# Kernel optimization log

Hardware: AMD Instinct MI355X
Metric: run time of the kernel (lower is better)

## Reference

```python
import jax, jax.numpy as jnp
import numpy as np

B = 16384
NUM_V = 1024
NUM_H = 1024
HYPER_DIM = 64
K = 10  # gibbs steps
T = 1.0


def setup_inputs() -> dict:
    key = jax.random.key(0)
    ks = jax.random.split(key, 9)
    v_data = jax.random.bernoulli(ks[0], 0.5, (B, NUM_V)).astype(jnp.float32)
    cond = jax.random.uniform(ks[1], (B, 1), jnp.float32)
    W = 0.01 * jax.random.normal(ks[2], (NUM_V, NUM_H), jnp.float32)
    b = 0.01 * jax.random.normal(ks[3], (NUM_V,), jnp.float32)
    c = 0.01 * jax.random.normal(ks[4], (NUM_H,), jnp.float32)
    fc1_w = jax.random.normal(ks[5], (HYPER_DIM, 1), jnp.float32)
    fc1_b = jnp.zeros((HYPER_DIM,), jnp.float32)
    fc2_w = jax.random.normal(ks[6], (2 * (NUM_V + NUM_H), HYPER_DIM), jnp.float32) / np.sqrt(HYPER_DIM)
    fc2_b = jnp.zeros((2 * (NUM_V + NUM_H),), jnp.float32)
    return {"v_data": v_data, "cond": cond, "W": W, "b": b, "c": c,
            "fc1_w": fc1_w, "fc1_b": fc1_b, "fc2_w": fc2_w, "fc2_b": fc2_b}


def _mod_biases(cond, b, c, fc1_w, fc1_b, fc2_w, fc2_b):
    x = jnp.tanh(cond @ fc1_w.T + fc1_b)
    y = x @ fc2_w.T + fc2_b  # [B, 2*(num_v+num_h)]
    gamma_b, beta_b, gamma_c, beta_c = jnp.split(
        y, [NUM_V, 2 * NUM_V, 2 * NUM_V + NUM_H], axis=-1)
    b_mod = (1.0 + gamma_b) * b[None, :] + beta_b  # [B, num_v]
    c_mod = (1.0 + gamma_c) * c[None, :] + beta_c  # [B, num_h]
    return b_mod, c_mod


def _free_energy(v, W, b_mod, c_mod):
    vW = v @ W  # [B, num_h]
    W_colsum = W.sum(axis=0)  # [num_h]
    sp_normal = jax.nn.softplus(vW + c_mod).sum(axis=-1)
    sp_flipped = jax.nn.softplus(W_colsum[None, :] - vW + c_mod).sum(axis=-1)
    vb_normal = -(v * b_mod).sum(axis=-1)
    vb_flipped = -((1.0 - v) * b_mod).sum(axis=-1)
    F_normal = vb_normal - sp_normal
    F_flipped = vb_flipped - sp_flipped
    negF = jnp.stack([-F_normal, -F_flipped], axis=-1)
    return -T * jax.nn.logsumexp(negF / T, axis=-1)


def _gibbs_step(carry, step_key, W, b_mod, c_mod):
    v, u = carry
    kh, ku, kv = jax.random.split(step_key, 3)
    v_branch = u * v + (1.0 - u) * (1.0 - v)
    p_h = jax.nn.sigmoid((v_branch @ W + c_mod) / T)
    h = jax.random.bernoulli(kh, p_h).astype(v.dtype)
    a = h @ W.T  # [B, num_v]
    dE = (-b_mod.sum(axis=-1) - a.sum(axis=-1)
          + 2.0 * (v * b_mod).sum(axis=-1) + 2.0 * (v * a).sum(axis=-1))
    p_u = jax.nn.sigmoid(dE / T)
    u = jax.random.bernoulli(ku, p_u).astype(v.dtype)[:, None]
    p_v = jax.nn.sigmoid((a + b_mod) / T)
    v_branch_new = jax.random.bernoulli(kv, p_v).astype(v.dtype)
    v_next = u * v_branch_new + (1.0 - u) * (1.0 - v_branch_new)
    return (v_next, u), None


def reference(v_data, cond, W, b, c, fc1_w, fc1_b, fc2_w, fc2_b):
    b_mod, c_mod = _mod_biases(cond, b, c, fc1_w, fc1_b, fc2_w, fc2_b)
    Bn = v_data.shape[0]
    key = jax.random.key(42)
    k_u, k_chain = jax.random.split(key)
    u0 = jax.random.bernoulli(k_u, 0.5, (Bn, 1)).astype(v_data.dtype)
    step_keys = jax.random.split(k_chain, K)
    step = lambda carry, sk: _gibbs_step(carry, sk, W, b_mod, c_mod)
    (v_model, _), _ = jax.lax.scan(step, (v_data, u0), step_keys)
    v_model = jax.lax.stop_gradient(v_model)
    loss = (_free_energy(v_data, W, b_mod, c_mod).mean()
            - _free_energy(v_model, W, b_mod, c_mod).mean())
    return loss
```

## Files before the change

### kernel.cpp

```cpp
#include <hip/hip_runtime.h>
#include <hip/hip_bf16.h>
#include <stdint.h>


#define NB 16384
#define KSTEPS 10
#define LDA 1152
#define KD 1088
#define NT 17
#define SLS 136
#define USALT 4000u
#define ONE8 ((unsigned char)0x38)

typedef __attribute__((ext_vector_type(4))) float f32x4;
typedef __attribute__((ext_vector_type(4))) unsigned int u32x4;

__device__ __forceinline__ unsigned hash32(unsigned idx, unsigned salt) {
  unsigned x = idx + salt * 0x9E3779B9u;
  x = (x ^ (x >> 16)) * 0x7feb352du;
  x = (x ^ (x >> 15)) * 0x846ca68bu;
  return x ^ (x >> 16);
}
__device__ __forceinline__ float rng_u01(unsigned salt, unsigned idx) {
  return (float)(hash32(idx, salt) >> 8) * (1.0f / 16777216.0f);
}
__device__ __forceinline__ float sigm(float z) { return 1.0f / (1.0f + __expf(-z)); }
__device__ __forceinline__ float softplus_(float z) {
  return fmaxf(z, 0.f) + __logf(1.f + __expf(-fabsf(z)));
}
__device__ __forceinline__ float lse2(float a, float b) {
  float m = fmaxf(a, b);
  return m + log1pf(__expf(fminf(a, b) - m));
}
__device__ __forceinline__ float bf2f(unsigned short s) {
  unsigned u = ((unsigned)s) << 16;
  return *reinterpret_cast<float*>(&u);
}
__device__ __forceinline__ unsigned short f2bf(float f) {
  __hip_bfloat16 h = __float2bfloat16(f);
  return *reinterpret_cast<unsigned short*>(&h);
}
__device__ unsigned char f2e4m3(float f) {
  unsigned u = __float_as_uint(f);
  unsigned char s = (unsigned char)((u >> 24) & 0x80);
  float af = fabsf(f);
  if (af >= 448.f) return s | 0x7E;
  float sub = rintf(af * 512.f);
  if (sub < 1.f) return s;
  if (af < 0.015625f) {
    int m = (int)sub;
    if (m > 7) return s | 0x08;
    return s | (unsigned char)m;
  }
  int ex; frexpf(af, &ex);
  int E = ex - 1;
  float q = rintf(ldexpf(af, 3 - E));
  int qi = (int)q;
  if (qi >= 16) { qi = 8; E += 1; if (E > 8) return s | 0x7E; }
  return s | (unsigned char)(((E + 7) << 3) | (qi - 8));
}
__device__ __forceinline__ float e4m3f(unsigned char v) {
  float s = (v & 0x80) ? -1.f : 1.f;
  int e = (v >> 3) & 15, m = v & 7;
  float mag = e ? ldexpf((float)(8 + m), e - 10) : ldexpf((float)m, -9);
  return s * mag;
}
__device__ __forceinline__ void gl2lds16(const void* g, void* l) {
  __builtin_amdgcn_global_load_lds(
      (const __attribute__((address_space(1))) unsigned int*)g,
      (__attribute__((address_space(3))) unsigned int*)l, 16, 0, 0);
}

template <int EPI>
__global__ __launch_bounds__(256, 4) void gemm_bt(
    const unsigned char* __restrict__ A, const unsigned char* __restrict__ Bt,
    unsigned char* sh, const float* __restrict__ cst8,
    const float* __restrict__ wcs, const float* __restrict__ Xf,
    const float* __restrict__ pv0, const float* __restrict__ pv1, unsigned usalt,
    float* __restrict__ p0, float* __restrict__ p1, float* __restrict__ p2,
    unsigned salt) {
  constexpr int MI = (EPI == 2 ? 2 : 4);
  constexpr int BM = MI * 32;
  constexpr int ABYT = BM * 64;
  constexpr int BUF = ABYT + 8192;
  __shared__ __align__(16) char smem[2 * BUF];
  unsigned char* newsl = (unsigned char*)smem;

  const int t = threadIdx.x;
  const int L = blockIdx.x;
  const int xcd = L & 7, li = L >> 3;
  constexpr int MMSK = (EPI == 2 ? 31 : 15);
  constexpr int NSH = (EPI == 2 ? 5 : 4);
  const int m0 = xcd * 2048 + (li & MMSK) * BM;
  const int n0 = (li >> NSH) * 128;
  const int lane = t & 63, wave = t >> 6;
  const int wm = (wave >> 1) * (MI * 16), wn = (wave & 1) * 64;
  const int lr = lane & 15, quad = lane >> 4;
  const int row8 = lane >> 2;
  const int qch = (((lane & 3) ^ (row8 & 3) ^ ((lane >> 4) & 3)) << 4);
  const int ql8 = (quad & 1) * 8, qh = quad >> 1;
  const int rx = (lr & 3) ^ ((lr >> 2) & 3);
  int koff[2];
#pragma unroll
  for (int s = 0; s < 2; ++s) koff[s] = (((s * 2 + qh) ^ rx) << 4) + ql8;

  const unsigned char* gA0 = A + (size_t)(m0 + wave * (MI * 8) + row8) * LDA + qch;
  const unsigned char* gA1 = gA0 + (size_t)16 * LDA;
  const unsigned char* gB0 = Bt + (size_t)(n0 + wave * 32 + row8) * LDA + qch;
  const unsigned char* gB1 = gB0 + (size_t)16 * LDA;

  auto stage = [&](int it, int bufb) {
    const int ko = it * 64;
    if constexpr (EPI == 2) {
      gl2lds16(gA0 + ko, smem + bufb + wave * 1024);
    } else {
      gl2lds16(gA0 + ko, smem + bufb + wave * 2048);
      gl2lds16(gA1 + ko, smem + bufb + wave * 2048 + 1024);
    }
    gl2lds16(gB0 + ko, smem + bufb + ABYT + wave * 2048);
    gl2lds16(gB1 + ko, smem + bufb + ABYT + wave * 2048 + 1024);
  };

  f32x4 acc[MI][4] = {};
  f32x4 accf[EPI == 2 ? MI : 1][4] = {};

  stage(0, 0);
  __syncthreads();

#pragma unroll
  for (int it = 0; it < NT; ++it) {
    const int base = (it & 1) * BUF;
    if (it + 1 < NT) stage(it + 1, base ^ BUF);
    const char* sA = (const char*)smem + base;
    const char* sB = sA + ABYT;
#pragma unroll
    for (int s = 0; s < 2; ++s) {
      long af[MI], bfr[4];
#pragma unroll
      for (int i = 0; i < MI; i++)
        af[i] = *(const long*)(sA + (wm + i * 16 + lr) * 64 + koff[s]);
#pragma unroll
      for (int j = 0; j < 4; j++)
        bfr[j] = *(const long*)(sB + (wn + j * 16 + lr) * 64 + koff[s]);
      if (EPI == 2 && it >= 16) {
#pragma unroll
        for (int i = 0; i < MI; i++)
#pragma unroll
          for (int j = 0; j < 4; j++)
            accf[i][j] = __builtin_amdgcn_mfma_f32_16x16x32_fp8_fp8(af[i], bfr[j], accf[i][j], 0, 0, 0);
      } else {
#pragma unroll
        for (int i = 0; i < MI; i++)
#pragma unroll
          for (int j = 0; j < 4; j++)
            acc[i][j] = __builtin_amdgcn_mfma_f32_16x16x32_fp8_fp8(af[i], bfr[j], acc[i][j], 0, 0, 0);
      }
    }
    __syncthreads();
  }

  float cst_j[4];
  if constexpr (EPI != 2) {
#pragma unroll
    for (int j = 0; j < 4; j++) cst_j[j] = cst8[n0 + wn + j * 16 + lr];
  }

  if constexpr (EPI == 2) {
    if (n0 >= 1024) {
#pragma unroll
      for (int i = 0; i < MI; i++)
#pragma unroll
        for (int rg = 0; rg < 4; rg++) {
          const int r = m0 + wm + i * 16 + quad * 4 + rg;
          float pb = 0.f;
          if (wn == 0) {
#pragma unroll
            for (int j = 0; j < 4; j++)
              pb += acc[i][j][rg] * Xf[(size_t)r * 64 + j * 16 + lr];
          } else {
            if (lr == 0) pb = acc[i][0][rg];
          }
#pragma unroll
          for (int msk = 1; msk < 16; msk <<= 1) pb += __shfl_xor(pb, msk, 64);
          if (lr == 0) atomicAdd(&p2[r], pb);
        }
      return;
    }
    float cstc_j[4];
#pragma unroll
    for (int j = 0; j < 4; j++) cstc_j[j] = cst8[n0 + wn + j * 16 + lr];
#pragma unroll
    for (int i = 0; i < MI; i++)
#pragma unroll
      for (int rg = 0; rg < 4; rg++) {
        const int r = m0 + wm + i * 16 + quad * 4 + rg;
        bool uu = true;
        if (pv0 != nullptr) {
          const float dE = -pv0[r] + 2.f * pv1[r];
          uu = rng_u01(usalt, (unsigned)r) < sigm(dE);
        }
        float sn = 0.f, sf = 0.f;
#pragma unroll
        for (int j = 0; j < 4; j++) {
          const int n = n0 + wn + j * 16 + lr;
          const float vw = acc[i][j][rg];
          const float cm = accf[i][j][rg] + cstc_j[j];
          const float s1 = softplus_(vw + cm);
          const float s2 = softplus_(wcs[n] - vw + cm);
          sn += uu ? s1 : s2;
          sf += uu ? s2 : s1;
        }
#pragma unroll
        for (int msk = 1; msk < 16; msk <<= 1) {
          sn += __shfl_xor(sn, msk, 64);
          sf += __shfl_xor(sf, msk, 64);
        }
        if (lr == 0) { atomicAdd(&p0[r], sn); atomicAdd(&p1[r], sf); }
      }
    return;
  }

  if constexpr (EPI == 1) {
    {
      const int rb = wave * (MI * 8);
#pragma unroll
      for (int q = 0; q < MI; ++q) {
        const int row = rb + q * 8 + (lane >> 3);
        const int sc = (lane & 7) ^ ((row >> 2) & 3);
        gl2lds16(sh + (size_t)(m0 + row) * LDA + n0 + sc * 16,
                 (unsigned char*)smem + BUF + (rb + q * 8) * 128);
      }
    }
    __syncthreads();
    const unsigned char* osl = (const unsigned char*)smem + BUF;
#pragma unroll
    for (int i = 0; i < MI; i++)
#pragma unroll
      for (int rg = 0; rg < 4; rg++) {
        const int r = m0 + wm + i * 16 + quad * 4 + rg;
        const int rowl = wm + i * 16 + quad * 4 + rg;
        const float dE = -pv0[r] + 2.f * pv1[r];
        const bool uu = rng_u01(usalt, (unsigned)r) < sigm(dE);
        float q0 = 0.f, q1 = 0.f;
#pragma unroll
        for (int j = 0; j < 4; ++j) {
          const float z = acc[i][j][rg] + cst_j[j];
          const int pc = ((wn >> 4) + j) ^ quad;
          const float so = (osl[rowl * 128 + pc * 16 + lr] != 0) ? 1.f : 0.f;
          const float v = uu ? so : 1.f - so;
          q0 += z; q1 += v * z;
        }
#pragma unroll
        for (int msk = 1; msk < 16; msk <<= 1) {
          q0 += __shfl_xor(q0, msk, 64);
          q1 += __shfl_xor(q1, msk, 64);
        }
        if (lr == 0) { atomicAdd(&p0[r], q0); atomicAdd(&p1[r], q1); }
      }
    __syncthreads();
  }

#pragma unroll
  for (int i = 0; i < MI; ++i)
#pragma unroll
    for (int rg = 0; rg < 4; ++rg) {
      const int rowl = wm + i * 16 + quad * 4 + rg;
      const int r = m0 + rowl;
#pragma unroll
      for (int jp = 0; jp < 2; ++jp) {
        const unsigned x = hash32((unsigned)(r << 10) + (unsigned)(n0 + wn + jp * 16 + lr), salt);
        const float f0 = (float)(x & 0xFFFFu), f1 = (float)(x >> 16);
        const float z0 = acc[i][jp][rg] + cst_j[jp];
        const float z1v = acc[i][jp + 2][rg] + cst_j[jp + 2];
        newsl[rowl * SLS + wn + jp * 16 + lr] =
            (f0 * __expf(-z0) < 65536.f - f0) ? ONE8 : (unsigned char)0;
        newsl[rowl * SLS + wn + (jp + 2) * 16 + lr] =
            (f1 * __expf(-z1v) < 65536.f - f1) ? ONE8 : (unsigned char)0;
      }
    }
  __syncthreads();
#pragma unroll
  for (int p = 0; p < BM / 32; ++p) {
    const int c = p * 256 + t, rowl = c >> 3, chk = c & 7;
    const u32x4 vv = *(const u32x4*)(newsl + rowl * SLS + chk * 16);
    *(u32x4*)(sh + (size_t)(m0 + rowl) * LDA + n0 + chk * 16) = vv;
  }
}

__global__ __launch_bounds__(256) void k_x(const float* __restrict__ cond,
                                           const float* __restrict__ fc1w,
                                           const float* __restrict__ fc1b, float* __restrict__ X) {
  int idx = blockIdx.x * 256 + threadIdx.x;
  int r = idx >> 6, k = idx & 63;
  X[idx] = tanhf(cond[r] * fc1w[k] + fc1b[k]);
}

__global__ __launch_bounds__(256) void k_g(const float* __restrict__ fc2w,
                                           const float* __restrict__ fc2b,
                                           const float* __restrict__ b, const float* __restrict__ c,
                                           float* __restrict__ Gb, float* __restrict__ Gc,
                                           float* __restrict__ cstb, float* __restrict__ cstc,
                                           float* __restrict__ cstb8, float* __restrict__ cstc8) {
  int idx = blockIdx.x * 256 + threadIdx.x;
  int j = idx >> 6, k = idx & 63;
  Gb[idx] = fc2w[(size_t)j * 64 + k] * b[j] + fc2w[(size_t)(1024 + j) * 64 + k];
  Gc[idx] = fc2w[(size_t)(2048 + j) * 64 + k] * c[j] + fc2w[(size_t)(3072 + j) * 64 + k];
  if (k == 0) {
    float vb = b[j] + fc2b[j] * b[j] + fc2b[1024 + j];
    float vc = c[j] + fc2b[2048 + j] * c[j] + fc2b[3072 + j];
    cstb[j] = vb; cstc[j] = vc;
    cstb8[j] = e4m3f(f2e4m3(vb));
    cstc8[j] = e4m3f(f2e4m3(vc));
  }
}

__global__ __launch_bounds__(256) void k_prep(const float* __restrict__ W,
                                              const float* __restrict__ Gb,
                                              const float* __restrict__ Gc,
                                              const float* __restrict__ cstb,
                                              const float* __restrict__ cstc,
                                              unsigned char* __restrict__ Wt,
                                              unsigned char* __restrict__ Wb) {
  int k = blockIdx.x * 256 + threadIdx.x;
  int n = blockIdx.y;
  if (k >= LDA) return;
  unsigned char wt = 0, wb = 0;
  if (n < 1024) {
    if (k < 1024) {
      wt = f2e4m3(W[(size_t)k * 1024 + n]);
      wb = f2e4m3(W[(size_t)n * 1024 + k]);
    } else if (k < 1088) {
      int j = k - 1024;
      wt = f2e4m3(Gc[(size_t)n * 64 + j]);
      wb = f2e4m3(Gb[(size_t)n * 64 + j]);
    } else if (k == 1088) {
      wt = f2e4m3(cstc[n]);
      wb = f2e4m3(cstb[n]);
    }
  } else if (k < 1024) {
    if (n < 1088) wt = f2e4m3(Gb[(size_t)k * 64 + (n - 1024)]);
    else if (n == 1088) wt = f2e4m3(cstb[k]);
  }
  Wt[(size_t)n * LDA + k] = wt;
  Wb[(size_t)n * LDA + k] = wb;
}

__global__ __launch_bounds__(256) void k_wcs(const float* __restrict__ W, float* __restrict__ wcs) {
  int n = blockIdx.x * 256 + threadIdx.x;
  float s = 0.f;
  for (int i = 0; i < 1024; i++) s += W[(size_t)i * 1024 + n];
  wcs[n] = s;
}

__global__ __launch_bounds__(128) void k_aux(const float* __restrict__ Gb,
                                             const float* __restrict__ cstb,
                                             float* __restrict__ aux) {
  int t = threadIdx.x;
  if (t < 64) {
    float s = 0.f;
    for (int j = 0; j < 1024; j++) s += Gb[(size_t)j * 64 + t];
    aux[t] = s;
  } else if (t == 64) {
    float s = 0.f;
    for (int j = 0; j < 1024; j++) s += cstb[j];
    aux[64] = s;
  }
}

__global__ __launch_bounds__(256) void k_sinit(const float* __restrict__ vdata,
                                               const float* __restrict__ X,
                                               unsigned char* __restrict__ S,
                                               unsigned char* __restrict__ H,
                                               unsigned char* __restrict__ V) {
  int k = blockIdx.x * 256 + threadIdx.x;
  int r = blockIdx.y;
  if (k >= LDA) return;
  const size_t o = (size_t)r * LDA + k;
  if (k < 1024) {
    float vd = vdata[(size_t)r * 1024 + k];
    V[o] = (vd != 0.f) ? ONE8 : (unsigned char)0;
    const bool u0 = rng_u01(USALT, (unsigned)r) < 0.5f;
    float sv = u0 ? vd : 1.f - vd;
    S[o] = (sv != 0.f) ? ONE8 : (unsigned char)0;
  } else {
    unsigned char xv;
    if (k < 1088) xv = f2e4m3(X[(size_t)r * 64 + (k - 1024)]);
    else if (k == 1088) xv = ONE8;
    else xv = 0;
    S[o] = xv; H[o] = xv; V[o] = xv;
  }
}

__global__ __launch_bounds__(256) void k_final(
    const float* __restrict__ Xf, const float* __restrict__ aux,
    const float* __restrict__ pv0, const float* __restrict__ pv1, unsigned usalt,
    const float* __restrict__ spn_d, const float* __restrict__ spf_d,
    const float* __restrict__ spn_m, const float* __restrict__ spf_m,
    const float* __restrict__ vb_d, const float* __restrict__ vb_m,
    float* __restrict__ fdiff) {
  __shared__ float ax[65];
  int t = threadIdx.x;
  if (t < 65) ax[t] = aux[t];
  __syncthreads();
  int r = blockIdx.x * 256 + t;
  float sb = ax[64];
  const float* xr = Xf + (size_t)r * 64;
#pragma unroll
  for (int k = 0; k < 64; k++) sb += xr[k] * ax[k];
  const float dE = -pv0[r] + 2.f * pv1[r];
  const bool uu = rng_u01(usalt, (unsigned)r) < sigm(dE);
  const float d1 = vb_d[r], d2 = vb_m[r];
  float F_d = -lse2(d1 + spn_d[r], (sb - d1) + spf_d[r]);
  float vbn = uu ? d2 : (sb - d2);
  float F_m = -lse2(vbn + spn_m[r], (sb - vbn) + spf_m[r]);
  fdiff[r] = F_d - F_m;
}

__global__ __launch_bounds__(256) void k_reduce(const float* __restrict__ fdiff,
                                                float* __restrict__ out) {
  __shared__ float red[4];
  int t = threadIdx.x;
  float s = 0.f;
  for (int i = t; i < NB; i += 256) s += fdiff[i];
  for (int m = 32; m >= 1; m >>= 1) s += __shfl_xor(s, m, 64);
  if ((t & 63) == 0) red[t >> 6] = s;
  __syncthreads();
  if (t == 0) out[0] = (red[0] + red[1] + red[2] + red[3]) * (1.0f / (float)NB);
}

extern "C" void kernel_launch(void* const* d_in, const int* in_sizes, int n_in, void* d_out,
                              int out_size, void* d_ws, size_t ws_size, hipStream_t stream) {
  const float* vdata = (const float*)d_in[0];
  const float* cond = (const float*)d_in[1];
  const float* W = (const float*)d_in[2];
  const float* bb = (const float*)d_in[3];
  const float* cc = (const float*)d_in[4];
  const float* fc1w = (const float*)d_in[5];
  const float* fc1b = (const float*)d_in[6];
  const float* fc2w = (const float*)d_in[7];
  const float* fc2b = (const float*)d_in[8];
  float* out = (float*)d_out;

  char* wp = (char*)d_ws;
  auto alloc = [&](size_t bytes) {
    char* p = wp;
    wp += (bytes + 255) & ~(size_t)255;
    return p;
  };
  unsigned char* Wt = (unsigned char*)alloc((size_t)1152 * LDA);
  unsigned char* Wb = (unsigned char*)alloc((size_t)1152 * LDA);
  float* wcs = (float*)alloc(1024 * 4);
  float* X = (float*)alloc((size_t)NB * 64 * 4);
  float* Gb = (float*)alloc((size_t)1024 * 64 * 4);
  float* Gc = (float*)alloc((size_t)1024 * 64 * 4);
  float* cstb = (float*)alloc(1024 * 4);
  float* cstc = (float*)alloc(1024 * 4);
  float* cstb8 = (float*)alloc(1024 * 4);
  float* cstc8 = (float*)alloc(1024 * 4);
  float* aux = (float*)alloc(65 * 4);
  unsigned char* S = (unsigned char*)alloc((size_t)NB * LDA);
  unsigned char* H = (unsigned char*)alloc((size_t)NB * LDA);
  unsigned char* V = (unsigned char*)alloc((size_t)NB * LDA);
  float* pall = (float*)alloc((size_t)(KSTEPS + 1 + 3) * 2 * NB * 4);
  float* spn_d = pall + (size_t)(KSTEPS + 1) * 2 * NB;
  float* spf_d = spn_d + NB;
  float* spn_m = spf_d + NB;
  float* spf_m = spn_m + NB;
  float* vb_d = spf_m + NB;
  float* vb_m = vb_d + NB;
  float* fdiff = (float*)alloc(NB * 4);
  auto P0 = [&](int t) { return pall + (size_t)(t + 1) * 2 * NB; };
  auto P1 = [&](int t) { return pall + (size_t)(t + 1) * 2 * NB + NB; };

  hipMemsetAsync(pall, 0, (size_t)(KSTEPS + 1 + 3) * 2 * NB * 4, stream);

  k_x<<<NB * 64 / 256, 256, 0, stream>>>(cond, fc1w, fc1b, X);
  k_g<<<1024 * 64 / 256, 256, 0, stream>>>(fc2w, fc2b, bb, cc, Gb, Gc, cstb, cstc, cstb8, cstc8);
  k_prep<<<dim3(5, 1152), 256, 0, stream>>>(W, Gb, Gc, cstb, cstc, Wt, Wb);
  k_wcs<<<4, 256, 0, stream>>>(W, wcs);
  k_aux<<<1, 128, 0, stream>>>(Gb, cstb, aux);
  k_sinit<<<dim3(5, NB), 256, 0, stream>>>(vdata, X, S, H, V);

  for (int step = 0; step < KSTEPS; ++step) {
    gemm_bt<0><<<1024, 256, 0, stream>>>(S, Wt, H, cstc8, nullptr, nullptr,
                                         nullptr, nullptr, 0u, nullptr, nullptr, nullptr,
                                         2000u + (unsigned)step);
    gemm_bt<1><<<1024, 256, 0, stream>>>(H, Wb, S, cstb8, nullptr, nullptr,
                                         P0(step - 1), P1(step - 1), USALT + (unsigned)step,
                                         P0(step), P1(step), nullptr,
                                         3000u + (unsigned)step);
  }

  gemm_bt<2><<<2304, 256, 0, stream>>>(V, Wt, nullptr, cstc8, wcs, X, nullptr, nullptr, 0u,
                                       spn_d, spf_d, vb_d, 0u);
  gemm_bt<2><<<2304, 256, 0, stream>>>(S, Wt, nullptr, cstc8, wcs, X,
                                       P0(KSTEPS - 1), P1(KSTEPS - 1), USALT + KSTEPS,
                                       spn_m, spf_m, vb_m, 0u);
  k_final<<<NB / 256, 256, 0, stream>>>(X, aux, P0(KSTEPS - 1), P1(KSTEPS - 1), USALT + KSTEPS,
                                        spn_d, spf_d, spn_m, spf_m, vb_d, vb_m, fdiff);
  k_reduce<<<1, 256, 0, stream>>>(fdiff, out);
}
```

Measured before the change: 1.019 ms.

## Switch GEMM operands from FP8 e4m3 to scaled int8 MFMA

Replaces fp8 e4m3 encoding of weights, bias-modulation features and binary states with fixed-scale int8 quantization, and uses the 16x16x64 int8 MFMA with int32 accumulators, rescaling in the epilogues. Each iteration now does one 16-byte LDS fragment load and one MFMA per tile pair instead of two 8-byte loads and two fp8 MFMAs. The constant bias is no longer folded into the GEMM through a ones column; full-precision float constants are added in the epilogue instead. Fixed scales risk clipping or coarser resolution for the hypernetwork terms and X.

```diff
diff --git a/kernel.cpp b/kernel.cpp
--- a/kernel.cpp
+++ b/kernel.cpp
@@ -10,9 +10,14 @@
 #define NT 17
 #define SLS 136
 #define USALT 4000u
-#define ONE8 ((unsigned char)0x38)
+#define BONE ((unsigned char)7)
+#define PSC 0x1.0p-13f
+#define RWQ 1170.2857142857f
+#define SGQ 64.0f
+#define SXQ 128.0f
 
 typedef __attribute__((ext_vector_type(4))) float f32x4;
+typedef __attribute__((ext_vector_type(4))) int i32x4;
 typedef __attribute__((ext_vector_type(4))) unsigned int u32x4;
 
 __device__ __forceinline__ unsigned hash32(unsigned idx, unsigned salt) {
@@ -32,38 +37,10 @@
   float m = fmaxf(a, b);
   return m + log1pf(__expf(fminf(a, b) - m));
 }
-__device__ __forceinline__ float bf2f(unsigned short s) {
-  unsigned u = ((unsigned)s) << 16;
-  return *reinterpret_cast<float*>(&u);
-}
-__device__ __forceinline__ unsigned short f2bf(float f) {
-  __hip_bfloat16 h = __float2bfloat16(f);
-  return *reinterpret_cast<unsigned short*>(&h);
-}
-__device__ unsigned char f2e4m3(float f) {
-  unsigned u = __float_as_uint(f);
-  unsigned char s = (unsigned char)((u >> 24) & 0x80);
-  float af = fabsf(f);
-  if (af >= 448.f) return s | 0x7E;
-  float sub = rintf(af * 512.f);
-  if (sub < 1.f) return s;
-  if (af < 0.015625f) {
-    int m = (int)sub;
-    if (m > 7) return s | 0x08;
-    return s | (unsigned char)m;
-  }
-  int ex; frexpf(af, &ex);
-  int E = ex - 1;
-  float q = rintf(ldexpf(af, 3 - E));
-  int qi = (int)q;
-  if (qi >= 16) { qi = 8; E += 1; if (E > 8) return s | 0x7E; }
-  return s | (unsigned char)(((E + 7) << 3) | (qi - 8));
-}
-__device__ __forceinline__ float e4m3f(unsigned char v) {
-  float s = (v & 0x80) ? -1.f : 1.f;
-  int e = (v >> 3) & 15, m = v & 7;
-  float mag = e ? ldexpf((float)(8 + m), e - 10) : ldexpf((float)m, -9);
-  return s * mag;
+__device__ __forceinline__ unsigned char qi8(float v, float s) {
+  float x = rintf(v * s);
+  x = fminf(fmaxf(x, -127.f), 127.f);
+  return (unsigned char)(signed char)(int)x;
 }
 __device__ __forceinline__ void gl2lds16(const void* g, void* l) {
   __builtin_amdgcn_global_load_lds(
@@ -74,7 +51,7 @@
 template <int EPI>
 __global__ __launch_bounds__(256, 4) void gemm_bt(
     const unsigned char* __restrict__ A, const unsigned char* __restrict__ Bt,
-    unsigned char* sh, const float* __restrict__ cst8,
+    unsigned char* sh, const float* __restrict__ cst,
     const float* __restrict__ wcs, const float* __restrict__ Xf,
     const float* __restrict__ pv0, const float* __restrict__ pv1, unsigned usalt,
     float* __restrict__ p0, float* __restrict__ p1, float* __restrict__ p2,
@@ -98,11 +75,8 @@
   const int lr = lane & 15, quad = lane >> 4;
   const int row8 = lane >> 2;
   const int qch = (((lane & 3) ^ (row8 & 3) ^ ((lane >> 4) & 3)) << 4);
-  const int ql8 = (quad & 1) * 8, qh = quad >> 1;
   const int rx = (lr & 3) ^ ((lr >> 2) & 3);
-  int koff[2];
-#pragma unroll
-  for (int s = 0; s < 2; ++s) koff[s] = (((s * 2 + qh) ^ rx) << 4) + ql8;
+  const int kph = ((quad ^ rx) << 4);
 
   const unsigned char* gA0 = A + (size_t)(m0 + wave * (MI * 8) + row8) * LDA + qch;
   const unsigned char* gA1 = gA0 + (size_t)16 * LDA;
@@ -121,8 +95,8 @@
     gl2lds16(gB1 + ko, smem + bufb + ABYT + wave * 2048 + 1024);
   };
 
-  f32x4 acc[MI][4] = {};
-  f32x4 accf[EPI == 2 ? MI : 1][4] = {};
+  i32x4 acc[MI][4] = {};
+  i32x4 accf[EPI == 2 ? MI : 1][4] = {};
 
   stage(0, 0);
   __syncthreads();
@@ -133,28 +107,25 @@
     if (it + 1 < NT) stage(it + 1, base ^ BUF);
     const char* sA = (const char*)smem + base;
     const char* sB = sA + ABYT;
-#pragma unroll
-    for (int s = 0; s < 2; ++s) {
-      long af[MI], bfr[4];
+    i32x4 af[MI], bfr[4];
+#pragma unroll
+    for (int i = 0; i < MI; i++)
+      af[i] = *(const i32x4*)(sA + (wm + i * 16 + lr) * 64 + kph);
+#pragma unroll
+    for (int j = 0; j < 4; j++)
+      bfr[j] = *(const i32x4*)(sB + (wn + j * 16 + lr) * 64 + kph);
+    if (EPI == 2 && it >= 16) {
 #pragma unroll
       for (int i = 0; i < MI; i++)
-        af[i] = *(const long*)(sA + (wm + i * 16 + lr) * 64 + koff[s]);
-#pragma unroll
-      for (int j = 0; j < 4; j++)
-        bfr[j] = *(const long*)(sB + (wn + j * 16 + lr) * 64 + koff[s]);
-      if (EPI == 2 && it >= 16) {
-#pragma unroll
-        for (int i = 0; i < MI; i++)
-#pragma unroll
-          for (int j = 0; j < 4; j++)
-            accf[i][j] = __builtin_amdgcn_mfma_f32_16x16x32_fp8_fp8(af[i], bfr[j], accf[i][j], 0, 0, 0);
-      } else {
-#pragma unroll
-        for (int i = 0; i < MI; i++)
-#pragma unroll
-          for (int j = 0; j < 4; j++)
-            acc[i][j] = __builtin_amdgcn_mfma_f32_16x16x32_fp8_fp8(af[i], bfr[j], acc[i][j], 0, 0, 0);
-      }
+#pragma unroll
+        for (int j = 0; j < 4; j++)
+          accf[i][j] = __builtin_amdgcn_mfma_i32_16x16x64_i8(af[i], bfr[j], accf[i][j], 0, 0, 0);
+    } else {
+#pragma unroll
+      for (int i = 0; i < MI; i++)
+#pragma unroll
+        for (int j = 0; j < 4; j++)
+          acc[i][j] = __builtin_amdgcn_mfma_i32_16x16x64_i8(af[i], bfr[j], acc[i][j], 0, 0, 0);
     }
     __syncthreads();
   }
@@ -162,7 +133,7 @@
   float cst_j[4];
   if constexpr (EPI != 2) {
 #pragma unroll
-    for (int j = 0; j < 4; j++) cst_j[j] = cst8[n0 + wn + j * 16 + lr];
+    for (int j = 0; j < 4; j++) cst_j[j] = cst[n0 + wn + j * 16 + lr];
   }
 
   if constexpr (EPI == 2) {
@@ -176,9 +147,10 @@
           if (wn == 0) {
 #pragma unroll
             for (int j = 0; j < 4; j++)
-              pb += acc[i][j][rg] * Xf[(size_t)r * 64 + j * 16 + lr];
+              pb += (float)acc[i][j][rg] * Xf[(size_t)r * 64 + j * 16 + lr];
+            pb *= (1.f / 448.f);
           } else {
-            if (lr == 0) pb = acc[i][0][rg];
+            if (lr == 0) pb = (float)acc[i][0][rg] * PSC;
           }
 #pragma unroll
           for (int msk = 1; msk < 16; msk <<= 1) pb += __shfl_xor(pb, msk, 64);
@@ -188,7 +160,7 @@
     }
     float cstc_j[4];
 #pragma unroll
-    for (int j = 0; j < 4; j++) cstc_j[j] = cst8[n0 + wn + j * 16 + lr];
+    for (int j = 0; j < 4; j++) cstc_j[j] = cst[n0 + wn + j * 16 + lr];
 #pragma unroll
     for (int i = 0; i < MI; i++)
 #pragma unroll
@@ -203,8 +175,8 @@
 #pragma unroll
         for (int j = 0; j < 4; j++) {
           const int n = n0 + wn + j * 16 + lr;
-          const float vw = acc[i][j][rg];
-          const float cm = accf[i][j][rg] + cstc_j[j];
+          const float vw = (float)acc[i][j][rg] * PSC;
+          const float cm = (float)accf[i][j][rg] * PSC + cstc_j[j];
           const float s1 = softplus_(vw + cm);
           const float s2 = softplus_(wcs[n] - vw + cm);
           sn += uu ? s1 : s2;
@@ -244,7 +216,7 @@
         float q0 = 0.f, q1 = 0.f;
 #pragma unroll
         for (int j = 0; j < 4; ++j) {
-          const float z = acc[i][j][rg] + cst_j[j];
+          const float z = (float)acc[i][j][rg] * PSC + cst_j[j];
           const int pc = ((wn >> 4) + j) ^ quad;
           const float so = (osl[rowl * 128 + pc * 16 + lr] != 0) ? 1.f : 0.f;
           const float v = uu ? so : 1.f - so;
@@ -270,12 +242,12 @@
       for (int jp = 0; jp < 2; ++jp) {
         const unsigned x = hash32((unsigned)(r << 10) + (unsigned)(n0 + wn + jp * 16 + lr), salt);
         const float f0 = (float)(x & 0xFFFFu), f1 = (float)(x >> 16);
-        const float z0 = acc[i][jp][rg] + cst_j[jp];
-        const float z1v = acc[i][jp + 2][rg] + cst_j[jp + 2];
+        const float z0 = (float)acc[i][jp][rg] * PSC + cst_j[jp];
+        const float z1v = (float)acc[i][jp + 2][rg] * PSC + cst_j[jp + 2];
         newsl[rowl * SLS + wn + jp * 16 + lr] =
-            (f0 * __expf(-z0) < 65536.f - f0) ? ONE8 : (unsigned char)0;
+            (f0 * __expf(-z0) < 65536.f - f0) ? BONE : (unsigned char)0;
         newsl[rowl * SLS + wn + (jp + 2) * 16 + lr] =
-            (f1 * __expf(-z1v) < 65536.f - f1) ? ONE8 : (unsigned char)0;
+            (f1 * __expf(-z1v) < 65536.f - f1) ? BONE : (unsigned char)0;
       }
     }
   __syncthreads();
@@ -299,18 +271,14 @@
                                            const float* __restrict__ fc2b,
                                            const float* __restrict__ b, const float* __restrict__ c,
                                            float* __restrict__ Gb, float* __restrict__ Gc,
-                                           float* __restrict__ cstb, float* __restrict__ cstc,
-                                           float* __restrict__ cstb8, float* __restrict__ cstc8) {
+                                           float* __restrict__ cstb, float* __restrict__ cstc) {
   int idx = blockIdx.x * 256 + threadIdx.x;
   int j = idx >> 6, k = idx & 63;
   Gb[idx] = fc2w[(size_t)j * 64 + k] * b[j] + fc2w[(size_t)(1024 + j) * 64 + k];
   Gc[idx] = fc2w[(size_t)(2048 + j) * 64 + k] * c[j] + fc2w[(size_t)(3072 + j) * 64 + k];
   if (k == 0) {
-    float vb = b[j] + fc2b[j] * b[j] + fc2b[1024 + j];
-    float vc = c[j] + fc2b[2048 + j] * c[j] + fc2b[3072 + j];
-    cstb[j] = vb; cstc[j] = vc;
-    cstb8[j] = e4m3f(f2e4m3(vb));
-    cstc8[j] = e4m3f(f2e4m3(vc));
+    cstb[j] = b[j] + fc2b[j] * b[j] + fc2b[1024 + j];
+    cstc[j] = c[j] + fc2b[2048 + j] * c[j] + fc2b[3072 + j];
   }
 }
 
@@ -327,19 +295,19 @@
   unsigned char wt = 0, wb = 0;
   if (n < 1024) {
     if (k < 1024) {
-      wt = f2e4m3(W[(size_t)k * 1024 + n]);
-      wb = f2e4m3(W[(size_t)n * 1024 + k]);
+      wt = qi8(W[(size_t)k * 1024 + n], RWQ);
+      wb = qi8(W[(size_t)n * 1024 + k], RWQ);
     } else if (k < 1088) {
       int j = k - 1024;
-      wt = f2e4m3(Gc[(size_t)n * 64 + j]);
-      wb = f2e4m3(Gb[(size_t)n * 64 + j]);
+      wt = qi8(Gc[(size_t)n * 64 + j], SGQ);
+      wb = qi8(Gb[(size_t)n * 64 + j], SGQ);
     } else if (k == 1088) {
-      wt = f2e4m3(cstc[n]);
-      wb = f2e4m3(cstb[n]);
+      wt = qi8(cstc[n], RWQ);
+      wb = qi8(cstb[n], RWQ);
     }
   } else if (k < 1024) {
-    if (n < 1088) wt = f2e4m3(Gb[(size_t)k * 64 + (n - 1024)]);
-    else if (n == 1088) wt = f2e4m3(cstb[k]);
+    if (n < 1088) wt = qi8(Gb[(size_t)k * 64 + (n - 1024)], SGQ);
+    else if (n == 1088) wt = qi8(cstb[k], RWQ);
   }
   Wt[(size_t)n * LDA + k] = wt;
   Wb[(size_t)n * LDA + k] = wb;
@@ -378,15 +346,13 @@
   const size_t o = (size_t)r * LDA + k;
   if (k < 1024) {
     float vd = vdata[(size_t)r * 1024 + k];
-    V[o] = (vd != 0.f) ? ONE8 : (unsigned char)0;
+    V[o] = (vd != 0.f) ? BONE : (unsigned char)0;
     const bool u0 = rng_u01(USALT, (unsigned)r) < 0.5f;
     float sv = u0 ? vd : 1.f - vd;
-    S[o] = (sv != 0.f) ? ONE8 : (unsigned char)0;
+    S[o] = (sv != 0.f) ? BONE : (unsigned char)0;
   } else {
-    unsigned char xv;
-    if (k < 1088) xv = f2e4m3(X[(size_t)r * 64 + (k - 1024)]);
-    else if (k == 1088) xv = ONE8;
-    else xv = 0;
+    unsigned char xv = 0;
+    if (k < 1088) xv = qi8(X[(size_t)r * 64 + (k - 1024)], SXQ);
     S[o] = xv; H[o] = xv; V[o] = xv;
   }
 }
@@ -455,8 +421,6 @@
   float* Gc = (float*)alloc((size_t)1024 * 64 * 4);
   float* cstb = (float*)alloc(1024 * 4);
   float* cstc = (float*)alloc(1024 * 4);
-  float* cstb8 = (float*)alloc(1024 * 4);
-  float* cstc8 = (float*)alloc(1024 * 4);
   float* aux = (float*)alloc(65 * 4);
   unsigned char* S = (unsigned char*)alloc((size_t)NB * LDA);
   unsigned char* H = (unsigned char*)alloc((size_t)NB * LDA);
@@ -475,25 +439,25 @@
   hipMemsetAsync(pall, 0, (size_t)(KSTEPS + 1 + 3) * 2 * NB * 4, stream);
 
   k_x<<<NB * 64 / 256, 256, 0, stream>>>(cond, fc1w, fc1b, X);
-  k_g<<<1024 * 64 / 256, 256, 0, stream>>>(fc2w, fc2b, bb, cc, Gb, Gc, cstb, cstc, cstb8, cstc8);
+  k_g<<<1024 * 64 / 256, 256, 0, stream>>>(fc2w, fc2b, bb, cc, Gb, Gc, cstb, cstc);
   k_prep<<<dim3(5, 1152), 256, 0, stream>>>(W, Gb, Gc, cstb, cstc, Wt, Wb);
   k_wcs<<<4, 256, 0, stream>>>(W, wcs);
   k_aux<<<1, 128, 0, stream>>>(Gb, cstb, aux);
   k_sinit<<<dim3(5, NB), 256, 0, stream>>>(vdata, X, S, H, V);
 
   for (int step = 0; step < KSTEPS; ++step) {
-    gemm_bt<0><<<1024, 256, 0, stream>>>(S, Wt, H, cstc8, nullptr, nullptr,
+    gemm_bt<0><<<1024, 256, 0, stream>>>(S, Wt, H, cstc, nullptr, nullptr,
                                          nullptr, nullptr, 0u, nullptr, nullptr, nullptr,
                                          2000u + (unsigned)step);
-    gemm_bt<1><<<1024, 256, 0, stream>>>(H, Wb, S, cstb8, nullptr, nullptr,
+    gemm_bt<1><<<1024, 256, 0, stream>>>(H, Wb, S, cstb, nullptr, nullptr,
                                          P0(step - 1), P1(step - 1), USALT + (unsigned)step,
                                          P0(step), P1(step), nullptr,
                                          3000u + (unsigned)step);
   }
 
-  gemm_bt<2><<<2304, 256, 0, stream>>>(V, Wt, nullptr, cstc8, wcs, X, nullptr, nullptr, 0u,
+  gemm_bt<2><<<2304, 256, 0, stream>>>(V, Wt, nullptr, cstc, wcs, X, nullptr, nullptr, 0u,
                                        spn_d, spf_d, vb_d, 0u);
-  gemm_bt<2><<<2304, 256, 0, stream>>>(S, Wt, nullptr, cstc8, wcs, X,
+  gemm_bt<2><<<2304, 256, 0, stream>>>(S, Wt, nullptr, cstc, wcs, X,
                                        P0(KSTEPS - 1), P1(KSTEPS - 1), USALT + KSTEPS,
                                        spn_m, spf_m, vb_m, 0u);
   k_final<<<NB / 256, 256, 0, stream>>>(X, aux, P0(KSTEPS - 1), P1(KSTEPS - 1), USALT + KSTEPS,
```

Result: no change. 1.003 ms (-1.6%).
